# Optimization experiments

Measured on AMD Instinct MI355X. Metric: run time of the kernel, lower is better.

Reference implementation:

```python
import jax, jax.numpy as jnp
import numpy as np

B = 16384
INPUT, HID, MEM, K = 512, 1024, 1152, 2
SQ = 48  # sqrt(MEM*K)
LN_EPS = 1e-5
P_EPS = 1e-12


def setup_inputs() -> dict:
    key = jax.random.key(0)
    ks = jax.random.split(key, 16)
    def lin(k, out_d, in_d):
        bound = 1.0 / np.sqrt(in_d)
        k1, k2 = jax.random.split(k)
        W = jax.random.uniform(k1, (out_d, in_d), jnp.float32, -bound, bound)
        b = jax.random.uniform(k2, (out_d,), jnp.float32, -bound, bound)
        return W, b
    W_h, b_h = lin(ks[0], HID, MEM + HID + INPUT)        # hmi2h
    W_a, b_a = lin(ks[1], K, MEM + HID)                   # hm2alpha
    W_b, b_b = lin(ks[2], K, MEM + HID)                   # hm2beta
    W_va, b_va = lin(ks[3], 2 * SQ, MEM + HID)            # hm2v_alpha
    W_vb, b_vb = lin(ks[4], 2 * SQ, MEM + HID)            # hm2v_beta
    return {
        "input": jax.random.normal(ks[5], (B, INPUT), jnp.float32),
        "h_prev": jax.random.normal(ks[6], (B, HID), jnp.float32),
        "m_prev": jax.random.normal(ks[7], (B, MEM), jnp.float32),
        "W_h": W_h, "b_h": b_h,
        "ln_g": jnp.ones((HID,), jnp.float32), "ln_b": jnp.zeros((HID,), jnp.float32),
        "W_a": W_a, "b_a": b_a, "W_b": W_b, "b_b": b_b,
        "W_va": W_va, "b_va": b_va, "W_vb": W_vb, "b_vb": b_vb,
    }


def _layernorm(x, g, b):
    mu = jnp.mean(x, axis=-1, keepdims=True)
    var = jnp.mean(jnp.square(x - mu), axis=-1, keepdims=True)
    return (x - mu) * jax.lax.rsqrt(var + LN_EPS) * g + b


def _outer_pnorm(hm, W, b):
    # u: [B, 2*SQ] -> outer product [B, SQ, SQ] -> view [B, K, MEM], p=5 normalize on last dim
    u = hm @ W.T + b
    u1, u2 = u[:, :SQ], u[:, SQ:]
    v = (u1[:, :, None] * u2[:, None, :]).reshape(-1, K, MEM)
    norm = jnp.sum(jnp.abs(v) ** 5, axis=2, keepdims=True) ** (1.0 / 5.0)
    return v / jnp.maximum(norm, P_EPS)


def reference(input, h_prev, m_prev, W_h, b_h, ln_g, ln_b, W_a, b_a, W_b, b_b, W_va, b_va, W_vb, b_vb):
    c = jnp.concatenate([input, h_prev, m_prev], axis=1)          # [B, INPUT+HID+MEM]
    h = jax.nn.relu(_layernorm(c @ W_h.T + b_h, ln_g, ln_b))      # [B, HID]
    hm = jnp.concatenate([h, m_prev], axis=1)                     # [B, HID+MEM]
    alpha = hm @ W_a.T + b_a                                      # [B, K] (use_relu=False)
    beta = hm @ W_b.T + b_b                                       # [B, K]
    v_alpha = _outer_pnorm(hm, W_va, b_va)                        # [B, K, MEM]
    v_beta = _outer_pnorm(hm, W_vb, b_vb)                         # [B, K, MEM]
    add_mem = jnp.mean(alpha[:, :, None] * v_alpha, axis=1)       # [B, MEM]
    forget_mem = jnp.mean(beta[:, :, None] * v_beta, axis=1)      # [B, MEM]
    m = m_prev + add_mem - forget_mem
    return h, m
```

## Files before the change

### kernel.cpp

```cpp
#include <hip/hip_runtime.h>
#include <hip/hip_bf16.h>
#include <cstdint>
#include <cstddef>

#define B_ROWS 16384
#define D_IN   512
#define D_HID  1024
#define D_MEM  1152
#define D_C    2688
#define D_HM   2176
#define N_U    224
#define N_U_REAL 196

typedef __attribute__((ext_vector_type(8))) short bf16x8;
typedef __attribute__((ext_vector_type(4))) float f32x4;

static __device__ __forceinline__ unsigned short f2bf(float f) {
  unsigned u = __float_as_uint(f);
  unsigned r = u + 0x7fffu + ((u >> 16) & 1u);
  return (unsigned short)(r >> 16);
}

#define GLOAD16(g, l) __builtin_amdgcn_global_load_lds( \
    (const __attribute__((address_space(1))) void*)(g), \
    (__attribute__((address_space(3))) void*)(l), 16, 0, 0)

__global__ __launch_bounds__(256) void pack_rows(
    const float* __restrict__ in, const float* __restrict__ hp,
    const float* __restrict__ mp,
    unsigned short* __restrict__ c, unsigned short* __restrict__ hm) {
  const int row = blockIdx.x;
  const int t = threadIdx.x;
  const float4* in4 = (const float4*)(in + (size_t)row * D_IN);
  const float4* hp4 = (const float4*)(hp + (size_t)row * D_HID);
  const float4* mp4 = (const float4*)(mp + (size_t)row * D_MEM);
  unsigned short* crow = c + (size_t)row * D_C;
  unsigned short* hrow = hm + (size_t)row * D_HM + D_HID;
  if (t < 128) {
    float4 v = in4[t];
    ushort4 o; o.x=f2bf(v.x); o.y=f2bf(v.y); o.z=f2bf(v.z); o.w=f2bf(v.w);
    *(ushort4*)(crow + t*4) = o;
  }
  {
    float4 v = hp4[t];
    ushort4 o; o.x=f2bf(v.x); o.y=f2bf(v.y); o.z=f2bf(v.z); o.w=f2bf(v.w);
    *(ushort4*)(crow + 512 + t*4) = o;
  }
  for (int i = t; i < 288; i += 256) {
    float4 v = mp4[i];
    ushort4 o; o.x=f2bf(v.x); o.y=f2bf(v.y); o.z=f2bf(v.z); o.w=f2bf(v.w);
    *(ushort4*)(crow + 1536 + i*4) = o;
    *(ushort4*)(hrow + i*4) = o;
  }
}

__global__ void conv_w4(const float* __restrict__ W, unsigned short* __restrict__ o, int n4) {
  for (int i = blockIdx.x*blockDim.x + threadIdx.x; i < n4; i += gridDim.x*blockDim.x) {
    float4 v = ((const float4*)W)[i];
    ushort4 u; u.x=f2bf(v.x); u.y=f2bf(v.y); u.z=f2bf(v.z); u.w=f2bf(v.w);
    ((ushort4*)o)[i] = u;
  }
}

__global__ void conv_wcat(const float* __restrict__ Wva, const float* __restrict__ Wvb,
                          const float* __restrict__ Wa, const float* __restrict__ Wb,
                          unsigned short* __restrict__ o) {
  const int n = N_U * D_HM;
  for (int i = blockIdx.x*blockDim.x + threadIdx.x; i < n; i += gridDim.x*blockDim.x) {
    int r = i / D_HM, col = i - r * D_HM;
    float v;
    if (r < 96)       v = Wva[r*D_HM + col];
    else if (r < 192) v = Wvb[(r-96)*D_HM + col];
    else if (r < 194) v = Wa[(r-192)*D_HM + col];
    else if (r < 196) v = Wb[(r-194)*D_HM + col];
    else              v = 0.f;
    o[i] = f2bf(v);
  }
}

__global__ __launch_bounds__(256, 2) void gemm1(
    const unsigned short* __restrict__ A,
    const unsigned short* __restrict__ W,
    float* __restrict__ Y) {
  __shared__ __align__(16) unsigned short As[128*32];
  __shared__ __align__(16) unsigned short Bs[128*32];
  const int tid  = threadIdx.x;
  const int lane = tid & 63;
  const int wave = tid >> 6;
  const int bm = blockIdx.x & 127;
  const int bn = blockIdx.x >> 7;
  const int wr = wave >> 1, wc = wave & 1;
  const int lr = lane & 15, kh = lane >> 4;

  f32x4 acc[4][4];
  #pragma unroll
  for (int i = 0; i < 4; ++i)
    #pragma unroll
    for (int j = 0; j < 4; ++j) acc[i][j] = (f32x4)(0.f);

  const unsigned short* Abase = A + (size_t)(bm*128) * D_C;
  const unsigned short* Wbase = W + (size_t)(bn*128) * D_C;
  const int s0 = tid, s1 = tid + 256;
  const int ar0 = s0 >> 2, ac0 = (s0 & 3) * 8;
  const int ar1 = s1 >> 2, ac1 = (s1 & 3) * 8;

  for (int k0 = 0; k0 < D_C; k0 += 32) {
    GLOAD16(Abase + (size_t)ar0*D_C + k0 + ac0, As + s0*8);
    GLOAD16(Abase + (size_t)ar1*D_C + k0 + ac1, As + s1*8);
    GLOAD16(Wbase + (size_t)ar0*D_C + k0 + ac0, Bs + s0*8);
    GLOAD16(Wbase + (size_t)ar1*D_C + k0 + ac1, Bs + s1*8);
    __syncthreads();
    bf16x8 a[4], b[4];
    #pragma unroll
    for (int mi = 0; mi < 4; ++mi)
      a[mi] = *(const bf16x8*)(As + (wr*64 + mi*16 + lr)*32 + kh*8);
    #pragma unroll
    for (int ni = 0; ni < 4; ++ni)
      b[ni] = *(const bf16x8*)(Bs + (wc*64 + ni*16 + lr)*32 + kh*8);
    #pragma unroll
    for (int mi = 0; mi < 4; ++mi)
      #pragma unroll
      for (int ni = 0; ni < 4; ++ni)
        acc[mi][ni] = __builtin_amdgcn_mfma_f32_16x16x32_bf16(a[mi], b[ni], acc[mi][ni], 0, 0, 0);
    __syncthreads();
  }
  const int orow0 = bm*128 + wr*64;
  const int ocol0 = bn*128 + wc*64;
  #pragma unroll
  for (int mi = 0; mi < 4; ++mi)
    #pragma unroll
    for (int ni = 0; ni < 4; ++ni)
      #pragma unroll
      for (int i = 0; i < 4; ++i) {
        int r  = orow0 + mi*16 + kh*4 + i;
        int cc = ocol0 + ni*16 + lr;
        Y[(size_t)r * D_HID + cc] = acc[mi][ni][i];
      }
}

__global__ __launch_bounds__(256) void ln_relu(
    float* __restrict__ Y, const float* __restrict__ bh,
    const float* __restrict__ g, const float* __restrict__ bb,
    unsigned short* __restrict__ hm) {
  const int row = blockIdx.x;
  const int t = threadIdx.x;
  float4 x = ((const float4*)(Y + (size_t)row * D_HID))[t];
  float4 b4 = ((const float4*)bh)[t];
  x.x += b4.x; x.y += b4.y; x.z += b4.z; x.w += b4.w;
  float s  = x.x + x.y + x.z + x.w;
  float sq = x.x*x.x + x.y*x.y + x.z*x.z + x.w*x.w;
  #pragma unroll
  for (int off = 32; off >= 1; off >>= 1) {
    s  += __shfl_down(s,  off, 64);
    sq += __shfl_down(sq, off, 64);
  }
  __shared__ float red[8];
  if ((t & 63) == 0) { red[t >> 6] = s; red[4 + (t >> 6)] = sq; }
  __syncthreads();
  float ts = red[0]+red[1]+red[2]+red[3];
  float tq = red[4]+red[5]+red[6]+red[7];
  float mu = ts * (1.f/1024.f);
  float var = tq * (1.f/1024.f) - mu*mu;
  float rstd = rsqrtf(var + 1e-5f);
  float4 g4  = ((const float4*)g)[t];
  float4 bb4 = ((const float4*)bb)[t];
  float4 o;
  o.x = fmaxf(0.f, (x.x - mu)*rstd*g4.x + bb4.x);
  o.y = fmaxf(0.f, (x.y - mu)*rstd*g4.y + bb4.y);
  o.z = fmaxf(0.f, (x.z - mu)*rstd*g4.z + bb4.z);
  o.w = fmaxf(0.f, (x.w - mu)*rstd*g4.w + bb4.w);
  ((float4*)(Y + (size_t)row * D_HID))[t] = o;
  ushort4 ob; ob.x=f2bf(o.x); ob.y=f2bf(o.y); ob.z=f2bf(o.z); ob.w=f2bf(o.w);
  *(ushort4*)(hm + (size_t)row * D_HM + t*4) = ob;
}

__global__ __launch_bounds__(512, 2) void gemm2(
    const unsigned short* __restrict__ A,
    const unsigned short* __restrict__ W,
    float* __restrict__ U) {
  __shared__ __align__(16) unsigned short As[64*32];
  __shared__ __align__(16) unsigned short Bs[224*32];
  const int tid  = threadIdx.x;
  const int lane = tid & 63;
  const int wave = tid >> 6;
  const int wr = wave >> 1, wc = wave & 1;
  const int lr = lane & 15, kh = lane >> 4;
  const int bm = blockIdx.x;

  f32x4 acc[7];
  #pragma unroll
  for (int i = 0; i < 7; ++i) acc[i] = (f32x4)(0.f);

  const unsigned short* Abase = A + (size_t)(bm*64) * D_HM;

  for (int k0 = 0; k0 < D_HM; k0 += 32) {
    if (tid < 256) {
      GLOAD16(Abase + (size_t)(tid>>2)*D_HM + k0 + (tid&3)*8, As + tid*8);
    } else {
      int sb = tid - 256;
      GLOAD16(W + (size_t)(sb>>2)*D_HM + k0 + (sb&3)*8, Bs + sb*8);
    }
    {
      int sb = tid + 256;
      GLOAD16(W + (size_t)(sb>>2)*D_HM + k0 + (sb&3)*8, Bs + sb*8);
    }
    if (tid < 128) {
      int sb = tid + 768;
      GLOAD16(W + (size_t)(sb>>2)*D_HM + k0 + (sb&3)*8, Bs + sb*8);
    }
    __syncthreads();
    bf16x8 a = *(const bf16x8*)(As + (wr*16 + lr)*32 + kh*8);
    #pragma unroll
    for (int ni = 0; ni < 7; ++ni) {
      bf16x8 b = *(const bf16x8*)(Bs + (wc*112 + ni*16 + lr)*32 + kh*8);
      acc[ni] = __builtin_amdgcn_mfma_f32_16x16x32_bf16(a, b, acc[ni], 0, 0, 0);
    }
    __syncthreads();
  }
  const int orow = bm*64 + wr*16 + kh*4;
  #pragma unroll
  for (int ni = 0; ni < 7; ++ni) {
    int cc = wc*112 + ni*16 + lr;
    #pragma unroll
    for (int i = 0; i < 4; ++i)
      U[(size_t)(orow + i) * N_U + cc] = acc[ni][i];
  }
}

__global__ __launch_bounds__(256) void gate(
    const float* __restrict__ U,
    const float* __restrict__ ba, const float* __restrict__ bbt,
    const float* __restrict__ bva, const float* __restrict__ bvb,
    const float* __restrict__ mp, float* __restrict__ Mo) {
  const int row = blockIdx.x;
  const int t = threadIdx.x;
  __shared__ float su[196];
  __shared__ float p5[192];
  __shared__ float S[6];
  __shared__ float coef[4];
  __shared__ float qa[24], qb[24];
  const float* urow = U + (size_t)row * N_U;
  if (t < 196) {
    float bias;
    if (t < 96)       bias = bva[t];
    else if (t < 192) bias = bvb[t - 96];
    else if (t < 194) bias = ba[t - 192];
    else              bias = bbt[t - 194];
    float v = urow[t] + bias;
    su[t] = v;
    if (t < 192) { float a = fabsf(v); p5[t] = a*a*a*a*a; }
  }
  __syncthreads();
  if (t < 6) {
    const int start[6] = {0, 24, 48, 96, 120, 144};
    const int cnt[6]   = {24, 24, 48, 24, 24, 48};
    float ssum = 0.f;
    for (int i = 0; i < cnt[t]; ++i) ssum += p5[start[t] + i];
    S[t] = ssum;
  }
  __syncthreads();
  if (t < 2) {
    float S2  = (t == 0) ? S[2] : S[5];
    float a0  = (t == 0) ? su[192] : su[194];
    float a1  = (t == 0) ? su[193] : su[195];
    float S10 = (t == 0) ? S[0] : S[3];
    float S11 = (t == 0) ? S[1] : S[4];
    float n0 = powf(S10 * S2, 0.2f);
    float n1 = powf(S11 * S2, 0.2f);
    coef[t*2 + 0] = 0.5f * a0 / fmaxf(n0, 1e-12f);
    coef[t*2 + 1] = 0.5f * a1 / fmaxf(n1, 1e-12f);
  }
  __syncthreads();
  if (t < 24)       qa[t]     = coef[0]*su[t]      + coef[1]*su[24 + t];
  else if (t < 48)  qb[t-24]  = coef[2]*su[96+t-24] + coef[3]*su[120 + t - 24];
  __syncthreads();
  const float4* mp4 = (const float4*)(mp + (size_t)row * D_MEM);
  float4*       mo4 = (float4*)(Mo + (size_t)row * D_MEM);
  for (int p4 = t; p4 < 288; p4 += 256) {
    float4 m = mp4[p4];
    int p = p4 * 4;
    int r = p / 48, c = p % 48;
    float A0 = qa[r], B0 = qb[r];
    float4 o;
    o.x = m.x + su[48 + c    ]*A0 - su[144 + c    ]*B0;
    o.y = m.y + su[48 + c + 1]*A0 - su[144 + c + 1]*B0;
    o.z = m.z + su[48 + c + 2]*A0 - su[144 + c + 2]*B0;
    o.w = m.w + su[48 + c + 3]*A0 - su[144 + c + 3]*B0;
    mo4[p4] = o;
  }
}

extern "C" void kernel_launch(void* const* d_in, const int* in_sizes, int n_in,
                              void* d_out, int out_size, void* d_ws, size_t ws_size,
                              hipStream_t stream) {
  const float* input  = (const float*)d_in[0];
  const float* h_prev = (const float*)d_in[1];
  const float* m_prev = (const float*)d_in[2];
  const float* W_h    = (const float*)d_in[3];
  const float* b_h    = (const float*)d_in[4];
  const float* ln_g   = (const float*)d_in[5];
  const float* ln_b   = (const float*)d_in[6];
  const float* W_a    = (const float*)d_in[7];
  const float* b_a    = (const float*)d_in[8];
  const float* W_b    = (const float*)d_in[9];
  const float* b_b    = (const float*)d_in[10];
  const float* W_va   = (const float*)d_in[11];
  const float* b_va   = (const float*)d_in[12];
  const float* W_vb   = (const float*)d_in[13];
  const float* b_vb   = (const float*)d_in[14];

  const size_t off_c    = 0;
  const size_t off_wh   = off_c    + (size_t)B_ROWS * D_C * 2;
  const size_t off_hm   = off_wh   + (size_t)D_HID * D_C * 2;
  const size_t off_wcat = off_hm   + (size_t)B_ROWS * D_HM * 2;
  const size_t off_U    = off_wcat + (size_t)N_U * D_HM * 2;
  const size_t need     = off_U    + (size_t)B_ROWS * N_U * 4;
  if (ws_size < need) return;

  char* ws = (char*)d_ws;
  unsigned short* c_bf  = (unsigned short*)(ws + off_c);
  unsigned short* wh_bf = (unsigned short*)(ws + off_wh);
  unsigned short* hm_bf = (unsigned short*)(ws + off_hm);
  unsigned short* wc_bf = (unsigned short*)(ws + off_wcat);
  float*          Ubuf  = (float*)(ws + off_U);

  float* h_out = (float*)d_out;
  float* m_out = h_out + (size_t)B_ROWS * D_HID;

  pack_rows<<<B_ROWS, 256, 0, stream>>>(input, h_prev, m_prev, c_bf, hm_bf);
  conv_w4  <<<1024, 256, 0, stream>>>(W_h, wh_bf, (D_HID * D_C) / 4);
  conv_wcat<<<1024, 256, 0, stream>>>(W_va, W_vb, W_a, W_b, wc_bf);
  gemm1    <<<1024, 256, 0, stream>>>(c_bf, wh_bf, h_out);
  ln_relu  <<<B_ROWS, 256, 0, stream>>>(h_out, b_h, ln_g, ln_b, hm_bf);
  gemm2    <<<B_ROWS / 64, 512, 0, stream>>>(hm_bf, wc_bf, Ubuf);
  gate     <<<B_ROWS, 256, 0, stream>>>(Ubuf, b_a, b_b, b_va, b_vb, m_prev, m_out);
}
```

Measured before the change: 530.2 us.

## Fuse fp32-to-bf16 input packing into both GEMM A-tile loads

Removes the pack_rows kernel and its bf16 concat buffers. gemm1 now reads input, h_prev and m_prev directly as fp32, converts them to bf16 in registers and stores them to LDS. gemm2 reads bf16 h from a dedicated buffer and converts m_prev from fp32 on the fly. gemm1's block index mapping also changes so that the 8 column blocks sharing an A row-tile run next to each other, which should help L2 reuse of the fp32 A reads. The intent is to avoid writing and re-reading the packed bf16 intermediates. The cost is that each A tile is now read as fp32 (twice the bytes), reread by all 8 column blocks, and converted redundantly, using synchronous register loads instead of async LDS loads.

```diff
diff --git a/kernel.cpp b/kernel.cpp
--- a/kernel.cpp
+++ b/kernel.cpp
@@ -10,7 +10,6 @@
 #define D_C    2688
 #define D_HM   2176
 #define N_U    224
-#define N_U_REAL 196
 
 typedef __attribute__((ext_vector_type(8))) short bf16x8;
 typedef __attribute__((ext_vector_type(4))) float f32x4;
@@ -24,35 +23,6 @@
 #define GLOAD16(g, l) __builtin_amdgcn_global_load_lds( \
     (const __attribute__((address_space(1))) void*)(g), \
     (__attribute__((address_space(3))) void*)(l), 16, 0, 0)
-
-__global__ __launch_bounds__(256) void pack_rows(
-    const float* __restrict__ in, const float* __restrict__ hp,
-    const float* __restrict__ mp,
-    unsigned short* __restrict__ c, unsigned short* __restrict__ hm) {
-  const int row = blockIdx.x;
-  const int t = threadIdx.x;
-  const float4* in4 = (const float4*)(in + (size_t)row * D_IN);
-  const float4* hp4 = (const float4*)(hp + (size_t)row * D_HID);
-  const float4* mp4 = (const float4*)(mp + (size_t)row * D_MEM);
-  unsigned short* crow = c + (size_t)row * D_C;
-  unsigned short* hrow = hm + (size_t)row * D_HM + D_HID;
-  if (t < 128) {
-    float4 v = in4[t];
-    ushort4 o; o.x=f2bf(v.x); o.y=f2bf(v.y); o.z=f2bf(v.z); o.w=f2bf(v.w);
-    *(ushort4*)(crow + t*4) = o;
-  }
-  {
-    float4 v = hp4[t];
-    ushort4 o; o.x=f2bf(v.x); o.y=f2bf(v.y); o.z=f2bf(v.z); o.w=f2bf(v.w);
-    *(ushort4*)(crow + 512 + t*4) = o;
-  }
-  for (int i = t; i < 288; i += 256) {
-    float4 v = mp4[i];
-    ushort4 o; o.x=f2bf(v.x); o.y=f2bf(v.y); o.z=f2bf(v.z); o.w=f2bf(v.w);
-    *(ushort4*)(crow + 1536 + i*4) = o;
-    *(ushort4*)(hrow + i*4) = o;
-  }
-}
 
 __global__ void conv_w4(const float* __restrict__ W, unsigned short* __restrict__ o, int n4) {
   for (int i = blockIdx.x*blockDim.x + threadIdx.x; i < n4; i += gridDim.x*blockDim.x) {
@@ -79,7 +49,8 @@
 }
 
 __global__ __launch_bounds__(256, 2) void gemm1(
-    const unsigned short* __restrict__ A,
+    const float* __restrict__ Xin, const float* __restrict__ Hp,
+    const float* __restrict__ Mp,
     const unsigned short* __restrict__ W,
     float* __restrict__ Y) {
   __shared__ __align__(16) unsigned short As[128*32];
@@ -87,8 +58,8 @@
   const int tid  = threadIdx.x;
   const int lane = tid & 63;
   const int wave = tid >> 6;
-  const int bm = blockIdx.x & 127;
-  const int bn = blockIdx.x >> 7;
+  const int bn = blockIdx.x & 7;
+  const int bm = blockIdx.x >> 3;
   const int wr = wave >> 1, wc = wave & 1;
   const int lr = lane & 15, kh = lane >> 4;
 
@@ -98,17 +69,30 @@
     #pragma unroll
     for (int j = 0; j < 4; ++j) acc[i][j] = (f32x4)(0.f);
 
-  const unsigned short* Abase = A + (size_t)(bm*128) * D_C;
   const unsigned short* Wbase = W + (size_t)(bn*128) * D_C;
   const int s0 = tid, s1 = tid + 256;
-  const int ar0 = s0 >> 2, ac0 = (s0 & 3) * 8;
-  const int ar1 = s1 >> 2, ac1 = (s1 & 3) * 8;
+  const int ar    = tid >> 1;
+  const int acoff = (tid & 1) * 16;
 
   for (int k0 = 0; k0 < D_C; k0 += 32) {
-    GLOAD16(Abase + (size_t)ar0*D_C + k0 + ac0, As + s0*8);
-    GLOAD16(Abase + (size_t)ar1*D_C + k0 + ac1, As + s1*8);
-    GLOAD16(Wbase + (size_t)ar0*D_C + k0 + ac0, Bs + s0*8);
-    GLOAD16(Wbase + (size_t)ar1*D_C + k0 + ac1, Bs + s1*8);
+    const float* src; int ld, kk;
+    if (k0 < 512)       { src = Xin; ld = D_IN;  kk = k0; }
+    else if (k0 < 1536) { src = Hp;  ld = D_HID; kk = k0 - 512; }
+    else                { src = Mp;  ld = D_MEM; kk = k0 - 1536; }
+    const float4* arow = (const float4*)(src + (size_t)(bm*128 + ar)*ld + kk + acoff);
+    float4 v0 = arow[0], v1 = arow[1], v2 = arow[2], v3 = arow[3];
+
+    GLOAD16(Wbase + (size_t)(s0>>2)*D_C + k0 + (s0&3)*8, Bs + s0*8);
+    GLOAD16(Wbase + (size_t)(s1>>2)*D_C + k0 + (s1&3)*8, Bs + s1*8);
+
+    bf16x8 p0, p1;
+    p0[0]=f2bf(v0.x); p0[1]=f2bf(v0.y); p0[2]=f2bf(v0.z); p0[3]=f2bf(v0.w);
+    p0[4]=f2bf(v1.x); p0[5]=f2bf(v1.y); p0[6]=f2bf(v1.z); p0[7]=f2bf(v1.w);
+    p1[0]=f2bf(v2.x); p1[1]=f2bf(v2.y); p1[2]=f2bf(v2.z); p1[3]=f2bf(v2.w);
+    p1[4]=f2bf(v3.x); p1[5]=f2bf(v3.y); p1[6]=f2bf(v3.z); p1[7]=f2bf(v3.w);
+    *(bf16x8*)(As + ar*32 + acoff)     = p0;
+    *(bf16x8*)(As + ar*32 + acoff + 8) = p1;
+
     __syncthreads();
     bf16x8 a[4], b[4];
     #pragma unroll
@@ -141,7 +125,7 @@
 __global__ __launch_bounds__(256) void ln_relu(
     float* __restrict__ Y, const float* __restrict__ bh,
     const float* __restrict__ g, const float* __restrict__ bb,
-    unsigned short* __restrict__ hm) {
+    unsigned short* __restrict__ hmh) {
   const int row = blockIdx.x;
   const int t = threadIdx.x;
   float4 x = ((const float4*)(Y + (size_t)row * D_HID))[t];
@@ -171,11 +155,12 @@
   o.w = fmaxf(0.f, (x.w - mu)*rstd*g4.w + bb4.w);
   ((float4*)(Y + (size_t)row * D_HID))[t] = o;
   ushort4 ob; ob.x=f2bf(o.x); ob.y=f2bf(o.y); ob.z=f2bf(o.z); ob.w=f2bf(o.w);
-  *(ushort4*)(hm + (size_t)row * D_HM + t*4) = ob;
+  *(ushort4*)(hmh + (size_t)row * D_HID + t*4) = ob;
 }
 
 __global__ __launch_bounds__(512, 2) void gemm2(
-    const unsigned short* __restrict__ A,
+    const unsigned short* __restrict__ Hb,
+    const float* __restrict__ Mp,
     const unsigned short* __restrict__ W,
     float* __restrict__ U) {
   __shared__ __align__(16) unsigned short As[64*32];
@@ -191,12 +176,25 @@
   #pragma unroll
   for (int i = 0; i < 7; ++i) acc[i] = (f32x4)(0.f);
 
-  const unsigned short* Abase = A + (size_t)(bm*64) * D_HM;
-
   for (int k0 = 0; k0 < D_HM; k0 += 32) {
-    if (tid < 256) {
-      GLOAD16(Abase + (size_t)(tid>>2)*D_HM + k0 + (tid&3)*8, As + tid*8);
+    if (k0 < 1024) {
+      if (tid < 256)
+        GLOAD16(Hb + (size_t)(bm*64 + (tid>>2))*D_HID + k0 + (tid&3)*8, As + tid*8);
     } else {
+      if (tid < 128) {
+        const int ar = tid >> 1, acoff = (tid & 1) * 16;
+        const float4* arow = (const float4*)(Mp + (size_t)(bm*64 + ar)*D_MEM + (k0-1024) + acoff);
+        float4 v0 = arow[0], v1 = arow[1], v2 = arow[2], v3 = arow[3];
+        bf16x8 p0, p1;
+        p0[0]=f2bf(v0.x); p0[1]=f2bf(v0.y); p0[2]=f2bf(v0.z); p0[3]=f2bf(v0.w);
+        p0[4]=f2bf(v1.x); p0[5]=f2bf(v1.y); p0[6]=f2bf(v1.z); p0[7]=f2bf(v1.w);
+        p1[0]=f2bf(v2.x); p1[1]=f2bf(v2.y); p1[2]=f2bf(v2.z); p1[3]=f2bf(v2.w);
+        p1[4]=f2bf(v3.x); p1[5]=f2bf(v3.y); p1[6]=f2bf(v3.z); p1[7]=f2bf(v3.w);
+        *(bf16x8*)(As + ar*32 + acoff)     = p0;
+        *(bf16x8*)(As + ar*32 + acoff + 8) = p1;
+      }
+    }
+    if (tid >= 256) {
       int sb = tid - 256;
       GLOAD16(W + (size_t)(sb>>2)*D_HM + k0 + (sb&3)*8, Bs + sb*8);
     }
@@ -271,7 +269,7 @@
     coef[t*2 + 1] = 0.5f * a1 / fmaxf(n1, 1e-12f);
   }
   __syncthreads();
-  if (t < 24)       qa[t]     = coef[0]*su[t]      + coef[1]*su[24 + t];
+  if (t < 24)       qa[t]     = coef[0]*su[t]       + coef[1]*su[24 + t];
   else if (t < 48)  qb[t-24]  = coef[2]*su[96+t-24] + coef[3]*su[120 + t - 24];
   __syncthreads();
   const float4* mp4 = (const float4*)(mp + (size_t)row * D_MEM);
@@ -300,38 +298,35 @@
   const float* b_h    = (const float*)d_in[4];
   const float* ln_g   = (const float*)d_in[5];
   const float* ln_b   = (const float*)d_in[6];
-  const float* W_a    = (const float*)d_in[7];
   const float* b_a    = (const float*)d_in[8];
   const float* W_b    = (const float*)d_in[9];
   const float* b_b    = (const float*)d_in[10];
+  const float* W_a    = (const float*)d_in[7];
   const float* W_va   = (const float*)d_in[11];
   const float* b_va   = (const float*)d_in[12];
   const float* W_vb   = (const float*)d_in[13];
   const float* b_vb   = (const float*)d_in[14];
 
-  const size_t off_c    = 0;
-  const size_t off_wh   = off_c    + (size_t)B_ROWS * D_C * 2;
-  const size_t off_hm   = off_wh   + (size_t)D_HID * D_C * 2;
-  const size_t off_wcat = off_hm   + (size_t)B_ROWS * D_HM * 2;
-  const size_t off_U    = off_wcat + (size_t)N_U * D_HM * 2;
+  const size_t off_wh   = 0;
+  const size_t off_wcat = off_wh   + (size_t)D_HID * D_C * 2;
+  const size_t off_hmh  = off_wcat + (size_t)N_U * D_HM * 2;
+  const size_t off_U    = off_hmh  + (size_t)B_ROWS * D_HID * 2;
   const size_t need     = off_U    + (size_t)B_ROWS * N_U * 4;
   if (ws_size < need) return;
 
   char* ws = (char*)d_ws;
-  unsigned short* c_bf  = (unsigned short*)(ws + off_c);
   unsigned short* wh_bf = (unsigned short*)(ws + off_wh);
-  unsigned short* hm_bf = (unsigned short*)(ws + off_hm);
   unsigned short* wc_bf = (unsigned short*)(ws + off_wcat);
+  unsigned short* hmh   = (unsigned short*)(ws + off_hmh);
   float*          Ubuf  = (float*)(ws + off_U);
 
   float* h_out = (float*)d_out;
   float* m_out = h_out + (size_t)B_ROWS * D_HID;
 
-  pack_rows<<<B_ROWS, 256, 0, stream>>>(input, h_prev, m_prev, c_bf, hm_bf);
   conv_w4  <<<1024, 256, 0, stream>>>(W_h, wh_bf, (D_HID * D_C) / 4);
   conv_wcat<<<1024, 256, 0, stream>>>(W_va, W_vb, W_a, W_b, wc_bf);
-  gemm1    <<<1024, 256, 0, stream>>>(c_bf, wh_bf, h_out);
-  ln_relu  <<<B_ROWS, 256, 0, stream>>>(h_out, b_h, ln_g, ln_b, hm_bf);
-  gemm2    <<<B_ROWS / 64, 512, 0, stream>>>(hm_bf, wc_bf, Ubuf);
+  gemm1    <<<1024, 256, 0, stream>>>(input, h_prev, m_prev, wh_bf, h_out);
+  ln_relu  <<<B_ROWS, 256, 0, stream>>>(h_out, b_h, ln_g, ln_b, hmh);
+  gemm2    <<<B_ROWS / 64, 512, 0, stream>>>(hmh, m_prev, wc_bf, Ubuf);
   gate     <<<B_ROWS, 256, 0, stream>>>(Ubuf, b_a, b_b, b_va, b_vb, m_prev, m_out);
 }
```

Result: slower. 585.1 us (+10.4%).

## Fuse gate epilogue into gemm2 and drop concatenated bf16 packing buffers

Applied to the files above, without the earlier changes.

Folds the per-row gating and p-norm computation into the gemm2 epilogue. The 224-wide projection tile now stays in LDS instead of being written to and re-read from a global U buffer. The input packing kernel is replaced by flat grid-stride conversions into separate x/h/m bf16 buffers, and both GEMMs pick their A source per K-segment. This avoids writing m twice and materializing the concatenated c/hm buffers. In exchange, gemm2 now uses about 73KB of LDS with one block per CU, which lowers occupancy.

```diff
diff --git a/kernel.cpp b/kernel.cpp
--- a/kernel.cpp
+++ b/kernel.cpp
@@ -10,7 +10,6 @@
 #define D_C    2688
 #define D_HM   2176
 #define N_U    224
-#define N_U_REAL 196
 
 typedef __attribute__((ext_vector_type(8))) short bf16x8;
 typedef __attribute__((ext_vector_type(4))) float f32x4;
@@ -25,32 +24,26 @@
     (const __attribute__((address_space(1))) void*)(g), \
     (__attribute__((address_space(3))) void*)(l), 16, 0, 0)
 
-__global__ __launch_bounds__(256) void pack_rows(
-    const float* __restrict__ in, const float* __restrict__ hp,
-    const float* __restrict__ mp,
-    unsigned short* __restrict__ c, unsigned short* __restrict__ hm) {
-  const int row = blockIdx.x;
-  const int t = threadIdx.x;
-  const float4* in4 = (const float4*)(in + (size_t)row * D_IN);
-  const float4* hp4 = (const float4*)(hp + (size_t)row * D_HID);
-  const float4* mp4 = (const float4*)(mp + (size_t)row * D_MEM);
-  unsigned short* crow = c + (size_t)row * D_C;
-  unsigned short* hrow = hm + (size_t)row * D_HM + D_HID;
-  if (t < 128) {
-    float4 v = in4[t];
+__global__ __launch_bounds__(256) void convert3(
+    const float* __restrict__ x, const float* __restrict__ h, const float* __restrict__ m,
+    unsigned short* __restrict__ xb, unsigned short* __restrict__ hb, unsigned short* __restrict__ mb) {
+  const int stride = gridDim.x * blockDim.x;
+  const int t0 = blockIdx.x * blockDim.x + threadIdx.x;
+  const int nx = B_ROWS * D_IN / 4, nh = B_ROWS * D_HID / 4, nm = B_ROWS * D_MEM / 4;
+  for (int i = t0; i < nx; i += stride) {
+    float4 v = ((const float4*)x)[i];
     ushort4 o; o.x=f2bf(v.x); o.y=f2bf(v.y); o.z=f2bf(v.z); o.w=f2bf(v.w);
-    *(ushort4*)(crow + t*4) = o;
-  }
-  {
-    float4 v = hp4[t];
+    ((ushort4*)xb)[i] = o;
+  }
+  for (int i = t0; i < nh; i += stride) {
+    float4 v = ((const float4*)h)[i];
     ushort4 o; o.x=f2bf(v.x); o.y=f2bf(v.y); o.z=f2bf(v.z); o.w=f2bf(v.w);
-    *(ushort4*)(crow + 512 + t*4) = o;
-  }
-  for (int i = t; i < 288; i += 256) {
-    float4 v = mp4[i];
+    ((ushort4*)hb)[i] = o;
+  }
+  for (int i = t0; i < nm; i += stride) {
+    float4 v = ((const float4*)m)[i];
     ushort4 o; o.x=f2bf(v.x); o.y=f2bf(v.y); o.z=f2bf(v.z); o.w=f2bf(v.w);
-    *(ushort4*)(crow + 1536 + i*4) = o;
-    *(ushort4*)(hrow + i*4) = o;
+    ((ushort4*)mb)[i] = o;
   }
 }
 
@@ -79,7 +72,9 @@
 }
 
 __global__ __launch_bounds__(256, 2) void gemm1(
-    const unsigned short* __restrict__ A,
+    const unsigned short* __restrict__ Xb,
+    const unsigned short* __restrict__ Hb,
+    const unsigned short* __restrict__ Mb,
     const unsigned short* __restrict__ W,
     float* __restrict__ Y) {
   __shared__ __align__(16) unsigned short As[128*32];
@@ -98,15 +93,18 @@
     #pragma unroll
     for (int j = 0; j < 4; ++j) acc[i][j] = (f32x4)(0.f);
 
-  const unsigned short* Abase = A + (size_t)(bm*128) * D_C;
   const unsigned short* Wbase = W + (size_t)(bn*128) * D_C;
   const int s0 = tid, s1 = tid + 256;
   const int ar0 = s0 >> 2, ac0 = (s0 & 3) * 8;
   const int ar1 = s1 >> 2, ac1 = (s1 & 3) * 8;
 
   for (int k0 = 0; k0 < D_C; k0 += 32) {
-    GLOAD16(Abase + (size_t)ar0*D_C + k0 + ac0, As + s0*8);
-    GLOAD16(Abase + (size_t)ar1*D_C + k0 + ac1, As + s1*8);
+    const unsigned short* asrc; int ald, akk;
+    if (k0 < 512)       { asrc = Xb; ald = D_IN;  akk = k0; }
+    else if (k0 < 1536) { asrc = Hb; ald = D_HID; akk = k0 - 512; }
+    else                { asrc = Mb; ald = D_MEM; akk = k0 - 1536; }
+    GLOAD16(asrc + (size_t)(bm*128 + ar0)*ald + akk + ac0, As + s0*8);
+    GLOAD16(asrc + (size_t)(bm*128 + ar1)*ald + akk + ac1, As + s1*8);
     GLOAD16(Wbase + (size_t)ar0*D_C + k0 + ac0, Bs + s0*8);
     GLOAD16(Wbase + (size_t)ar1*D_C + k0 + ac1, Bs + s1*8);
     __syncthreads();
@@ -141,7 +139,7 @@
 __global__ __launch_bounds__(256) void ln_relu(
     float* __restrict__ Y, const float* __restrict__ bh,
     const float* __restrict__ g, const float* __restrict__ bb,
-    unsigned short* __restrict__ hm) {
+    unsigned short* __restrict__ hmh) {
   const int row = blockIdx.x;
   const int t = threadIdx.x;
   float4 x = ((const float4*)(Y + (size_t)row * D_HID))[t];
@@ -171,15 +169,26 @@
   o.w = fmaxf(0.f, (x.w - mu)*rstd*g4.w + bb4.w);
   ((float4*)(Y + (size_t)row * D_HID))[t] = o;
   ushort4 ob; ob.x=f2bf(o.x); ob.y=f2bf(o.y); ob.z=f2bf(o.z); ob.w=f2bf(o.w);
-  *(ushort4*)(hm + (size_t)row * D_HM + t*4) = ob;
-}
-
-__global__ __launch_bounds__(512, 2) void gemm2(
-    const unsigned short* __restrict__ A,
+  *(ushort4*)(hmh + (size_t)row * D_HID + t*4) = ob;
+}
+
+__global__ __launch_bounds__(512, 1) void gemm2g(
+    const unsigned short* __restrict__ Hb,
+    const unsigned short* __restrict__ Mb,
     const unsigned short* __restrict__ W,
-    float* __restrict__ U) {
-  __shared__ __align__(16) unsigned short As[64*32];
-  __shared__ __align__(16) unsigned short Bs[224*32];
+    const float* __restrict__ ba, const float* __restrict__ bbt,
+    const float* __restrict__ bva, const float* __restrict__ bvb,
+    const float* __restrict__ mp,
+    float* __restrict__ Mo) {
+  __shared__ __align__(16) char smem[896 + 57344 + 2048 + 1024 + 12288];
+  float*          bias_s = (float*)smem;
+  unsigned short* As     = (unsigned short*)(smem + 896);
+  unsigned short* Bs     = (unsigned short*)(smem + 896 + 4096);
+  float*          Us     = (float*)(smem + 896);
+  float*          sm_s   = (float*)(smem + 896 + 57344);
+  float*          coef_s = (float*)(smem + 896 + 57344 + 2048);
+  float*          q_s    = (float*)(smem + 896 + 57344 + 3072);
+
   const int tid  = threadIdx.x;
   const int lane = tid & 63;
   const int wave = tid >> 6;
@@ -187,16 +196,28 @@
   const int lr = lane & 15, kh = lane >> 4;
   const int bm = blockIdx.x;
 
+  if (tid < N_U) {
+    int c = tid; float v;
+    if (c < 96)       v = bva[c];
+    else if (c < 192) v = bvb[c - 96];
+    else if (c < 194) v = ba[c - 192];
+    else if (c < 196) v = bbt[c - 194];
+    else              v = 0.f;
+    bias_s[c] = v;
+  }
+
   f32x4 acc[7];
   #pragma unroll
   for (int i = 0; i < 7; ++i) acc[i] = (f32x4)(0.f);
 
-  const unsigned short* Abase = A + (size_t)(bm*64) * D_HM;
-
   for (int k0 = 0; k0 < D_HM; k0 += 32) {
     if (tid < 256) {
-      GLOAD16(Abase + (size_t)(tid>>2)*D_HM + k0 + (tid&3)*8, As + tid*8);
-    } else {
+      const unsigned short* asrc; int ald, akk;
+      if (k0 < 1024) { asrc = Hb; ald = D_HID; akk = k0; }
+      else           { asrc = Mb; ald = D_MEM; akk = k0 - 1024; }
+      GLOAD16(asrc + (size_t)(bm*64 + (tid>>2))*ald + akk + (tid&3)*8, As + tid*8);
+    }
+    if (tid >= 256) {
       int sb = tid - 256;
       GLOAD16(W + (size_t)(sb>>2)*D_HM + k0 + (sb&3)*8, Bs + sb*8);
     }
@@ -217,76 +238,80 @@
     }
     __syncthreads();
   }
-  const int orow = bm*64 + wr*16 + kh*4;
-  #pragma unroll
-  for (int ni = 0; ni < 7; ++ni) {
-    int cc = wc*112 + ni*16 + lr;
-    #pragma unroll
-    for (int i = 0; i < 4; ++i)
-      U[(size_t)(orow + i) * N_U + cc] = acc[ni][i];
-  }
-}
-
-__global__ __launch_bounds__(256) void gate(
-    const float* __restrict__ U,
-    const float* __restrict__ ba, const float* __restrict__ bbt,
-    const float* __restrict__ bva, const float* __restrict__ bvb,
-    const float* __restrict__ mp, float* __restrict__ Mo) {
-  const int row = blockIdx.x;
-  const int t = threadIdx.x;
-  __shared__ float su[196];
-  __shared__ float p5[192];
-  __shared__ float S[6];
-  __shared__ float coef[4];
-  __shared__ float qa[24], qb[24];
-  const float* urow = U + (size_t)row * N_U;
-  if (t < 196) {
-    float bias;
-    if (t < 96)       bias = bva[t];
-    else if (t < 192) bias = bvb[t - 96];
-    else if (t < 194) bias = ba[t - 192];
-    else              bias = bbt[t - 194];
-    float v = urow[t] + bias;
-    su[t] = v;
-    if (t < 192) { float a = fabsf(v); p5[t] = a*a*a*a*a; }
-  }
-  __syncthreads();
-  if (t < 6) {
-    const int start[6] = {0, 24, 48, 96, 120, 144};
-    const int cnt[6]   = {24, 24, 48, 24, 24, 48};
+
+  {
+    const int row = wr*16 + kh*4;
+    #pragma unroll
+    for (int ni = 0; ni < 7; ++ni) {
+      int cc = wc*112 + ni*16 + lr;
+      float bb4 = bias_s[cc];
+      #pragma unroll
+      for (int i = 0; i < 4; ++i)
+        Us[(row + i)*N_U + cc] = acc[ni][i] + bb4;
+    }
+  }
+  __syncthreads();
+
+  const int gr = tid >> 3;
+  const int gj = tid & 7;
+  {
+    const float* su = Us + gr*N_U;
     float ssum = 0.f;
-    for (int i = 0; i < cnt[t]; ++i) ssum += p5[start[t] + i];
-    S[t] = ssum;
-  }
-  __syncthreads();
-  if (t < 2) {
-    float S2  = (t == 0) ? S[2] : S[5];
-    float a0  = (t == 0) ? su[192] : su[194];
-    float a1  = (t == 0) ? su[193] : su[195];
-    float S10 = (t == 0) ? S[0] : S[3];
-    float S11 = (t == 0) ? S[1] : S[4];
-    float n0 = powf(S10 * S2, 0.2f);
-    float n1 = powf(S11 * S2, 0.2f);
-    coef[t*2 + 0] = 0.5f * a0 / fmaxf(n0, 1e-12f);
-    coef[t*2 + 1] = 0.5f * a1 / fmaxf(n1, 1e-12f);
-  }
-  __syncthreads();
-  if (t < 24)       qa[t]     = coef[0]*su[t]      + coef[1]*su[24 + t];
-  else if (t < 48)  qb[t-24]  = coef[2]*su[96+t-24] + coef[3]*su[120 + t - 24];
-  __syncthreads();
-  const float4* mp4 = (const float4*)(mp + (size_t)row * D_MEM);
-  float4*       mo4 = (float4*)(Mo + (size_t)row * D_MEM);
-  for (int p4 = t; p4 < 288; p4 += 256) {
-    float4 m = mp4[p4];
-    int p = p4 * 4;
-    int r = p / 48, c = p % 48;
-    float A0 = qa[r], B0 = qb[r];
-    float4 o;
-    o.x = m.x + su[48 + c    ]*A0 - su[144 + c    ]*B0;
-    o.y = m.y + su[48 + c + 1]*A0 - su[144 + c + 1]*B0;
-    o.z = m.z + su[48 + c + 2]*A0 - su[144 + c + 2]*B0;
-    o.w = m.w + su[48 + c + 3]*A0 - su[144 + c + 3]*B0;
-    mo4[p4] = o;
+    #pragma unroll 4
+    for (int i = 0; i < 24; ++i) {
+      float a = fabsf(su[gj*24 + i]);
+      float a2 = a*a;
+      ssum += a2*a2*a;
+    }
+    sm_s[gr*8 + gj] = ssum;
+  }
+  __syncthreads();
+  if (gj == 0) {
+    const float* sm = sm_s + gr*8;
+    const float* su = Us + gr*N_U;
+    float S2a = sm[2] + sm[3];
+    float S2b = sm[6] + sm[7];
+    float n0 = powf(sm[0]*S2a, 0.2f);
+    float n1 = powf(sm[1]*S2a, 0.2f);
+    float n2 = powf(sm[4]*S2b, 0.2f);
+    float n3 = powf(sm[5]*S2b, 0.2f);
+    coef_s[gr*4+0] = 0.5f * su[192] / fmaxf(n0, 1e-12f);
+    coef_s[gr*4+1] = 0.5f * su[193] / fmaxf(n1, 1e-12f);
+    coef_s[gr*4+2] = 0.5f * su[194] / fmaxf(n2, 1e-12f);
+    coef_s[gr*4+3] = 0.5f * su[195] / fmaxf(n3, 1e-12f);
+  }
+  __syncthreads();
+  {
+    const float* su = Us + gr*N_U;
+    const float* cf = coef_s + gr*4;
+    #pragma unroll
+    for (int i = 0; i < 6; ++i) {
+      int mq = gj*6 + i;
+      float v;
+      if (mq < 24) v = cf[0]*su[mq]        + cf[1]*su[24 + mq];
+      else         v = cf[2]*su[96 + mq-24] + cf[3]*su[120 + mq-24];
+      q_s[gr*48 + mq] = v;
+    }
+  }
+  __syncthreads();
+  {
+    const float4* mp4 = (const float4*)(mp + (size_t)(bm*64) * D_MEM);
+    float4*       mo4 = (float4*)(Mo + (size_t)(bm*64) * D_MEM);
+    for (int idx = tid; idx < 64*288; idx += 512) {
+      int row = idx / 288;
+      int p4  = idx - row*288;
+      int p = p4*4;
+      int rr = p/48, c = p - rr*48;
+      const float* su = Us + row*N_U;
+      float A0 = q_s[row*48 + rr], B0 = q_s[row*48 + 24 + rr];
+      float4 m = mp4[row*288 + p4];
+      float4 o;
+      o.x = m.x + su[48 + c    ]*A0 - su[144 + c    ]*B0;
+      o.y = m.y + su[48 + c + 1]*A0 - su[144 + c + 1]*B0;
+      o.z = m.z + su[48 + c + 2]*A0 - su[144 + c + 2]*B0;
+      o.w = m.w + su[48 + c + 3]*A0 - su[144 + c + 3]*B0;
+      mo4[row*288 + p4] = o;
+    }
   }
 }
 
@@ -309,29 +334,30 @@
   const float* W_vb   = (const float*)d_in[13];
   const float* b_vb   = (const float*)d_in[14];
 
-  const size_t off_c    = 0;
-  const size_t off_wh   = off_c    + (size_t)B_ROWS * D_C * 2;
-  const size_t off_hm   = off_wh   + (size_t)D_HID * D_C * 2;
-  const size_t off_wcat = off_hm   + (size_t)B_ROWS * D_HM * 2;
-  const size_t off_U    = off_wcat + (size_t)N_U * D_HM * 2;
-  const size_t need     = off_U    + (size_t)B_ROWS * N_U * 4;
+  const size_t off_wh   = 0;
+  const size_t off_wcat = off_wh   + (size_t)D_HID * D_C * 2;
+  const size_t off_xb   = off_wcat + (size_t)N_U * D_HM * 2;
+  const size_t off_hb   = off_xb   + (size_t)B_ROWS * D_IN * 2;
+  const size_t off_mb   = off_hb   + (size_t)B_ROWS * D_HID * 2;
+  const size_t off_hmh  = off_mb   + (size_t)B_ROWS * D_MEM * 2;
+  const size_t need     = off_hmh  + (size_t)B_ROWS * D_HID * 2;
   if (ws_size < need) return;
 
   char* ws = (char*)d_ws;
-  unsigned short* c_bf  = (unsigned short*)(ws + off_c);
   unsigned short* wh_bf = (unsigned short*)(ws + off_wh);
-  unsigned short* hm_bf = (unsigned short*)(ws + off_hm);
   unsigned short* wc_bf = (unsigned short*)(ws + off_wcat);
-  float*          Ubuf  = (float*)(ws + off_U);
+  unsigned short* xb    = (unsigned short*)(ws + off_xb);
+  unsigned short* hb    = (unsigned short*)(ws + off_hb);
+  unsigned short* mb    = (unsigned short*)(ws + off_mb);
+  unsigned short* hmh   = (unsigned short*)(ws + off_hmh);
 
   float* h_out = (float*)d_out;
   float* m_out = h_out + (size_t)B_ROWS * D_HID;
 
-  pack_rows<<<B_ROWS, 256, 0, stream>>>(input, h_prev, m_prev, c_bf, hm_bf);
+  convert3 <<<2048, 256, 0, stream>>>(input, h_prev, m_prev, xb, hb, mb);
   conv_w4  <<<1024, 256, 0, stream>>>(W_h, wh_bf, (D_HID * D_C) / 4);
-  conv_wcat<<<1024, 256, 0, stream>>>(W_va, W_vb, W_a, W_b, wc_bf);
-  gemm1    <<<1024, 256, 0, stream>>>(c_bf, wh_bf, h_out);
-  ln_relu  <<<B_ROWS, 256, 0, stream>>>(h_out, b_h, ln_g, ln_b, hm_bf);
-  gemm2    <<<B_ROWS / 64, 512, 0, stream>>>(hm_bf, wc_bf, Ubuf);
-  gate     <<<B_ROWS, 256, 0, stream>>>(Ubuf, b_a, b_b, b_va, b_vb, m_prev, m_out);
-}
+  conv_wcat<<<256, 256, 0, stream>>>(W_va, W_vb, W_a, W_b, wc_bf);
+  gemm1    <<<1024, 256, 0, stream>>>(xb, hb, mb, wh_bf, h_out);
+  ln_relu  <<<B_ROWS, 256, 0, stream>>>(h_out, b_h, ln_g, ln_b, hmh);
+  gemm2g   <<<B_ROWS / 64, 512, 0, stream>>>(hmh, mb, wc_bf, b_a, b_b, b_va, b_vb, m_prev, m_out);
+}
```

New measurement: 504.7 us. 1.05x faster.
